# Kernel optimization log

Measured on AMD Instinct MI355X. Metric: run time of the kernel, lower is better.

Reference implementation:

```python
import jax, jax.numpy as jnp
import numpy as np

T, B, N, KALL, F, ORD, DIN, H, NH, HD, DE, DOUT = 4, 4, 16384, 4, 16384, 3, 4, 64, 4, 16, 4, 64


def setup_inputs() -> dict:
    key = jax.random.key(0)
    ks = jax.random.split(key, 32)
    p = lambda k, shape: (jax.random.normal(k, shape) * 0.1).astype(jnp.float32)
    indices = jax.random.randint(ks[0], (F, ORD), 0, N, dtype=jnp.int32)
    cnt = jnp.zeros((N,), jnp.float32).at[indices.reshape(-1)].add(1.0)
    nnz = jnp.maximum(cnt, 1.0)  # per-node nonzero count (avoid div-by-zero)
    return {
        "h": p(ks[1], (B, N, H)),
        "h_global": p(ks[2], (B, KALL, DOUT)),
        "x": p(ks[3], (T, B, N, DIN)),
        "extra": p(ks[4], (T, B, KALL, DE)),
        "dones": jax.random.bernoulli(ks[5], 0.1, (T, B)),
        "indices": indices,
        "nnz": nnz,
        # GRU cell params (flax GRUCell layout: i-dense with bias, h-dense no bias except n-gate)
        "Wi": p(ks[6], (DIN, 3 * H)), "bi": p(ks[7], (3 * H,)),
        "Wh": p(ks[8], (H, 3 * H)), "bhn": p(ks[9], (H,)),
        # MultiHeadAttention params
        "Wq": p(ks[10], (H, NH, HD)), "bq": p(ks[11], (NH, HD)),
        "Wk": p(ks[12], (H, NH, HD)), "bk": p(ks[13], (NH, HD)),
        "Wv": p(ks[14], (H, NH, HD)), "bv": p(ks[15], (NH, HD)),
        "Wo": p(ks[16], (NH, HD, H)), "bo": p(ks[17], (H,)),
        # output MLP (logit head) and value head
        "W1": p(ks[18], (H + DE, DOUT)), "b1": p(ks[19], (DOUT,)),
        "W2": p(ks[20], (DOUT, 1)), "b2": p(ks[21], (1,)),
        "Wv1": p(ks[22], (H + DE, 1)), "bv1": p(ks[23], (1,)),
    }


def reference(h, h_global, x, extra, dones, indices, nnz,
              Wi, bi, Wh, bhn, Wq, bq, Wk, bk, Wv, bv, Wo, bo,
              W1, b1, W2, b2, Wv1, bv1):
    Hd = Wh.shape[0]

    def gru_step(carry, inp):
        xt, dt = inp  # xt: [B,N,din], dt: [B]
        c = jnp.where(dt[:, None, None], jnp.zeros_like(carry), carry)
        gi = xt @ Wi + bi          # [B,N,3H]
        gh = c @ Wh                # [B,N,3H]
        r = jax.nn.sigmoid(gi[..., :Hd] + gh[..., :Hd])
        z = jax.nn.sigmoid(gi[..., Hd:2 * Hd] + gh[..., Hd:2 * Hd])
        n = jnp.tanh(gi[..., 2 * Hd:] + r * (gh[..., 2 * Hd:] + bhn))
        new = (1.0 - z) * n + z * c
        return new, new

    h_fin, hs = jax.lax.scan(gru_step, h, (x, dones))  # hs: [T,B,N,H]

    # gather per-factor neighbor hidden states
    g = jnp.take(hs, indices, axis=2)  # [T,B,F,ord,H]
    q = jnp.einsum('tbfkh,hnd->tbfknd', g, Wq) + bq
    kk = jnp.einsum('tbfkh,hnd->tbfknd', g, Wk) + bk
    vv = jnp.einsum('tbfkh,hnd->tbfknd', g, Wv) + bv
    scale = 1.0 / np.sqrt(q.shape[-1]).astype(np.float32)
    att = jax.nn.softmax(jnp.einsum('tbfqnd,tbfknd->tbfnqk', q * scale, kk), axis=-1)
    o = jnp.einsum('tbfnqk,tbfknd->tbfqnd', att, vv)
    a = jnp.einsum('tbfknd,ndh->tbfkh', o, Wo) + bo  # [T,B,F,ord,H]

    Tn, Bn = a.shape[0], a.shape[1]
    Nn = nnz.shape[0]
    a_flat = a.reshape(Tn, Bn, -1, a.shape[-1])  # [T,B,F*ord,H]
    # segment-sum scatter back to nodes, normalized by nnz
    y = jnp.zeros((Tn, Bn, Nn, a.shape[-1]), a.dtype).at[:, :, indices.reshape(-1), :].add(a_flat)
    y = y / nnz[None, None, :, None]

    Kall = extra.shape[2]
    N0 = Nn // Kall
    ypi = y.reshape(Tn, Bn, Kall, N0, y.shape[-1])
    y_global = jnp.mean(ypi, axis=3)                       # [T,B,K,H]
    z_global = jnp.concatenate((y_global, extra), axis=3)  # [T,B,K,H+DE]
    extra_t = jnp.broadcast_to(extra[:, :, :, None, :], (Tn, Bn, Kall, N0, extra.shape[-1]))
    z = jnp.concatenate((ypi, extra_t), axis=4).reshape(Tn, Bn, Nn, -1)
    value = (z_global @ Wv1 + bv1).sum(axis=2)             # [T,B,1]
    logit = (jax.nn.relu(z @ W1 + b1) @ W2 + b2).squeeze(axis=3)  # [T,B,N]
    return h_fin, h_global, logit, value.squeeze(axis=-1)
```

## Files before the change

### kernel.cpp

```cpp
#include <hip/hip_runtime.h>
#include <hip/hip_bf16.h>

#define T_ 4
#define B_ 4
#define N_ 16384
#define KALL_ 4
#define F_ 16384
#define ORD_ 3
#define DIN_ 4
#define H_ 64
#define H3_ 192
#define DE_ 4
#define STR 72
#define NE_ 49152

typedef __attribute__((ext_vector_type(8))) short s16x8;
typedef __attribute__((ext_vector_type(4))) float f32x4;
typedef __attribute__((ext_vector_type(2))) float f32x2;
typedef unsigned long long u64;

static __device__ __forceinline__ float b2f(unsigned short u) {
  union { unsigned u; float f; } x; x.u = ((unsigned)u) << 16; return x.f;
}
static __device__ __forceinline__ unsigned short f2b(float f) {
  __hip_bfloat16 h = __float2bfloat16(f);
  union { __hip_bfloat16 h; unsigned short u; } x; x.h = h; return x.u;
}
static __device__ __forceinline__ float sigm_fast(float v) {
  return __builtin_amdgcn_rcpf(1.f + __expf(-v));
}
static __device__ __forceinline__ float tanh_fast(float v) {
  float e = __expf(2.f * v);
  return 1.f - 2.f * __builtin_amdgcn_rcpf(e + 1.f);
}

__global__ __launch_bounds__(256) void k_csr_count(
    const int* __restrict__ idx, int* __restrict__ cnt) {
  int e = blockIdx.x * 256 + threadIdx.x;
  if (e < NE_) atomicAdd(&cnt[idx[e]], 1);
}
__global__ __launch_bounds__(256) void k_csr_scan(
    const int* __restrict__ cnt, int* __restrict__ offs, int* __restrict__ cursor) {
  __shared__ int part[256];
  __shared__ int base[256];
  int t = threadIdx.x;
  int s = 0;
  for (int j = 0; j < 64; ++j) s += cnt[t * 64 + j];
  part[t] = s;
  __syncthreads();
  if (t == 0) {
    int run = 0;
    for (int i = 0; i < 256; ++i) { base[i] = run; run += part[i]; }
  }
  __syncthreads();
  int run = base[t];
  for (int j = 0; j < 64; ++j) {
    offs[t * 64 + j] = run;
    cursor[t * 64 + j] = run;
    run += cnt[t * 64 + j];
  }
  if (t == 255) offs[N_] = run;
}
__global__ __launch_bounds__(256) void k_csr_fill(
    const int* __restrict__ idx, int* __restrict__ cursor, int* __restrict__ elist) {
  int e = blockIdx.x * 256 + threadIdx.x;
  if (e < NE_) {
    int pos = atomicAdd(&cursor[idx[e]], 1);
    elist[pos] = e;
  }
}

__global__ __launch_bounds__(256) void k_prep_wh(
    const float* __restrict__ Wh, unsigned short* __restrict__ whTg) {
  int i = blockIdx.x * 256 + threadIdx.x;
  int rr = i >> 6, k = i & 63;
  int ct = rr >> 4, c = rr & 15;
  int g = ct >> 2, cg = ct & 3;
  whTg[i] = f2b(Wh[k * H3_ + g * 64 + 4 * c + cg]);
}

__global__ __launch_bounds__(256) void k_prep_wa(
    const float* __restrict__ Wq, const float* __restrict__ Wk,
    const float* __restrict__ Wv, const float* __restrict__ Wo,
    unsigned short* __restrict__ wT) {
  int i = blockIdx.x * 256 + threadIdx.x;
  int m = i >> 12, col = (i >> 6) & 63, k = i & 63;
  const float* Wm = (m == 0) ? Wq : (m == 1) ? Wk : (m == 2) ? Wv : Wo;
  wT[i] = f2b(Wm[k * 64 + col]);
}

__global__ __launch_bounds__(256) void k_gru(
    const float* __restrict__ h0,
    const float* __restrict__ x,
    const int* __restrict__ dones,
    const unsigned short* __restrict__ whTg,
    const float* __restrict__ Wi,
    const float* __restrict__ bi,
    const float* __restrict__ bhn,
    unsigned short* __restrict__ hs,
    float* __restrict__ hfin)
{
  __shared__ __align__(16) short whT[H3_ * 72];
  __shared__ __align__(16) short carry[H_ * 72];
  __shared__ float wiS[5 * H3_];

  const int tid = threadIdx.x;
  const int lane = tid & 63;
  const int w = tid >> 6;
  const int c15 = lane & 15;
  const int hi4 = lane >> 4;
  const int bid = blockIdx.x;
  const int b = bid >> 8;
  const int nbase = (bid & 255) * 64;
  const int hb = 4 * c15;

#pragma unroll
  for (int c = 0; c < 6; ++c) {
    int lin = (c * 256 + tid) * 8;
    int row = lin >> 6, col = lin & 63;
    *(s16x8*)&whT[row * 72 + col] = *(const s16x8*)&whTg[lin];
  }
  for (int i = tid; i < 5 * H3_; i += 256)
    wiS[i] = (i < 4 * H3_) ? Wi[i] : bi[i - 4 * H3_];

  f32x4 cf[4];
#pragma unroll
  for (int r = 0; r < 4; ++r) {
    int row = 16 * w + 4 * hi4 + r;
    cf[r] = *(const f32x4*)&h0[(size_t)(b * N_ + nbase + row) * H_ + hb];
    u64 pk = 0;
#pragma unroll
    for (int e = 0; e < 4; ++e) pk |= (u64)f2b(cf[r][e]) << (16 * e);
    *(u64*)&carry[row * 72 + hb] = pk;
  }

  float bhnr[4];
#pragma unroll
  for (int cg = 0; cg < 4; ++cg) bhnr[cg] = bhn[hb + cg];

  unsigned dmask = 0;
  {
    bool word = true;
#pragma unroll
    for (int i = 0; i < 16; ++i) {
      int v = dones[i];
      if (v != 0 && v != 1 && v != 0x3F800000) word = false;
    }
#pragma unroll
    for (int t = 0; t < T_; ++t) {
      int tb = t * B_ + b;
      bool d = word ? (dones[tb] != 0) : (((const unsigned char*)dones)[tb] != 0);
      if (d) dmask |= (1u << t);
    }
  }

  __syncthreads();

  const int rowA = 16 * w + c15;
  for (int t = 0; t < T_; ++t) {
    if ((dmask >> t) & 1u) {
#pragma unroll
      for (int r = 0; r < 4; ++r) {
        cf[r] = (f32x4){0.f, 0.f, 0.f, 0.f};
        *(u64*)&carry[(16 * w + 4 * hi4 + r) * 72 + hb] = 0ull;
      }
    }

    s16x8 af0 = *(const s16x8*)&carry[rowA * 72 + hi4 * 8];
    s16x8 af1 = *(const s16x8*)&carry[rowA * 72 + 32 + hi4 * 8];

    f32x4 xv[4];
#pragma unroll
    for (int r = 0; r < 4; ++r) {
      const int node = nbase + 16 * w + 4 * hi4 + r;
      xv[r] = *(const f32x4*)&x[(size_t)((t * B_ + b) * N_ + node) * DIN_];
    }

#pragma unroll
    for (int hh = 0; hh < 2; ++hh) {
      f32x4 acc[6];
#pragma unroll
      for (int j = 0; j < 6; ++j) acc[j] = (f32x4){0.f, 0.f, 0.f, 0.f};
#pragma unroll
      for (int j = 0; j < 6; ++j) {
        const int ct = (j >> 1) * 4 + 2 * hh + (j & 1);
        acc[j] = __builtin_amdgcn_mfma_f32_16x16x32_bf16(
            af0, *(const s16x8*)&whT[(16 * ct + c15) * 72 + hi4 * 8], acc[j], 0, 0, 0);
      }
#pragma unroll
      for (int j = 0; j < 6; ++j) {
        const int ct = (j >> 1) * 4 + 2 * hh + (j & 1);
        acc[j] = __builtin_amdgcn_mfma_f32_16x16x32_bf16(
            af1, *(const s16x8*)&whT[(16 * ct + c15) * 72 + 32 + hi4 * 8], acc[j], 0, 0, 0);
      }
      const int hb2 = hb + 2 * hh;
#pragma unroll
      for (int r = 0; r < 4; ++r) {
        f32x2 gi[3];
#pragma unroll
        for (int g = 0; g < 3; ++g) {
          f32x2 s = *(const f32x2*)&wiS[4 * H3_ + g * 64 + hb2];
#pragma unroll
          for (int kk = 0; kk < 4; ++kk) {
            f32x2 wv = *(const f32x2*)&wiS[kk * H3_ + g * 64 + hb2];
            s += xv[r][kk] * wv;
          }
          gi[g] = s;
        }
#pragma unroll
        for (int c2 = 0; c2 < 2; ++c2) {
          const int cg = 2 * hh + c2;
          float rg = sigm_fast(gi[0][c2] + acc[c2][r]);
          float zg = sigm_fast(gi[1][c2] + acc[2 + c2][r]);
          float ng = tanh_fast(gi[2][c2] + rg * (acc[4 + c2][r] + bhnr[cg]));
          float nc = zg * (cf[r][cg] - ng) + ng;
          cf[r][cg] = nc;
        }
      }
    }

#pragma unroll
    for (int r = 0; r < 4; ++r) {
      const int row = 16 * w + 4 * hi4 + r;
      const int node = nbase + row;
      u64 pk = 0;
#pragma unroll
      for (int e = 0; e < 4; ++e) pk |= (u64)f2b(cf[r][e]) << (16 * e);
      *(u64*)&hs[(size_t)((t * B_ + b) * N_ + node) * H_ + hb] = pk;
      *(u64*)&carry[row * 72 + hb] = pk;
      if (t == T_ - 1)
        *(f32x4*)&hfin[(size_t)(b * N_ + node) * H_ + hb] = cf[r];
    }
  }
}

__global__ __launch_bounds__(256) void k_attn(
    const int tb0,
    const unsigned short* __restrict__ hs,
    const int* __restrict__ indices,
    const unsigned short* __restrict__ wT,
    const float* __restrict__ bq, const float* __restrict__ bk,
    const float* __restrict__ bv, const float* __restrict__ bo,
    unsigned short* __restrict__ a_edge)
{
  __shared__ __align__(16) unsigned short bufrag[3072];
  __shared__ __align__(8)  unsigned short qkvs[9792];
  __shared__ float biasf[4][64];
  __shared__ int idxs[48];

  const int tid = threadIdx.x;
  const int lane = tid & 63;
  const int w = tid >> 6;
  const int c15 = lane & 15;
  const int hi4 = lane >> 4;
  const int bid = blockIdx.x;
  const int slice = bid >> 10;
  const int fch = bid & 1023;
  const int col = 16 * w + c15;
  const int swz = (c15 ^ (hi4 << 2));

  if (tid < 48) idxs[tid] = indices[fch * 48 + tid];
  if (tid < 64) {
    biasf[0][tid] = bq[tid];
    biasf[1][tid] = bk[tid];
    biasf[2][tid] = bv[tid];
    biasf[3][tid] = bo[tid];
  }

  s16x8 wB[3][2], wB3[2];
#pragma unroll
  for (int m = 0; m < 3; ++m)
#pragma unroll
    for (int ks = 0; ks < 2; ++ks)
      wB[m][ks] = *(const s16x8*)&wT[(m * 64 + col) * 64 + ks * 32 + hi4 * 8];
#pragma unroll
  for (int ks = 0; ks < 2; ++ks)
    wB3[ks] = *(const s16x8*)&wT[(3 * 64 + col) * 64 + ks * 32 + hi4 * 8];
  __syncthreads();

  const size_t hbase = (size_t)(tb0 + slice) * N_;
  u64 pf[3];
#pragma unroll
  for (int k = 0; k < 3; ++k) {
    int idx = k * 256 + tid, row = idx >> 4, g = idx & 15;
    pf[k] = *(const u64*)&hs[(hbase + idxs[row]) * H_ + g * 4];
  }
#pragma unroll
  for (int k = 0; k < 3; ++k) {
    int idx = k * 256 + tid, row = idx >> 4, g = idx & 15;
    int rt = row >> 4, cr = row & 15;
    int ks = g >> 3, h5 = (g >> 1) & 3, j = (g & 1) * 4;
    int cr2 = cr ^ (h5 << 2);
    *(u64*)&bufrag[((rt * 2 + ks) << 9) + ((h5 * 16 + cr2) << 3) + j] = pf[k];
  }
  __syncthreads();

  s16x8 afr[3][2];
#pragma unroll
  for (int rt = 0; rt < 3; ++rt)
#pragma unroll
    for (int ks = 0; ks < 2; ++ks)
      afr[rt][ks] = *(const s16x8*)&bufrag[((rt * 2 + ks) << 9) + ((hi4 * 16 + swz) << 3)];
#pragma unroll
  for (int m = 0; m < 3; ++m) {
    float bias = biasf[m][col];
    float scl = (m == 0) ? 0.25f : 1.f;
#pragma unroll
    for (int rt = 0; rt < 3; ++rt) {
      f32x4 acc = (f32x4){0.f, 0.f, 0.f, 0.f};
      acc = __builtin_amdgcn_mfma_f32_16x16x32_bf16(afr[rt][0], wB[m][0], acc, 0, 0, 0);
      acc = __builtin_amdgcn_mfma_f32_16x16x32_bf16(afr[rt][1], wB[m][1], acc, 0, 0, 0);
#pragma unroll
      for (int r = 0; r < 4; ++r) {
        int row = 16 * rt + hi4 * 4 + r;
        qkvs[m * 3264 + row * 68 + col] = f2b((acc[r] + bias) * scl);
      }
    }
  }
  __syncthreads();

  {
    int f = tid >> 4, head = (tid >> 2) & 3, dq = tid & 3;
    int colb = head * 16 + dq * 4;
    float qv[3][4], kv[3][4], vv[3][4];
#pragma unroll
    for (int qi = 0; qi < 3; ++qi) {
      int base = (3 * f + qi) * 68 + colb;
      u64 uq = *(const u64*)&qkvs[base];
      u64 uk = *(const u64*)&qkvs[3264 + base];
      u64 uv = *(const u64*)&qkvs[6528 + base];
#pragma unroll
      for (int e = 0; e < 4; ++e) {
        qv[qi][e] = b2f((unsigned short)(uq >> (16 * e)));
        kv[qi][e] = b2f((unsigned short)(uk >> (16 * e)));
        vv[qi][e] = b2f((unsigned short)(uv >> (16 * e)));
      }
    }
    float s[3][3];
#pragma unroll
    for (int qi = 0; qi < 3; ++qi)
#pragma unroll
      for (int ki = 0; ki < 3; ++ki) {
        float a = qv[qi][0] * kv[ki][0] + qv[qi][1] * kv[ki][1]
                + qv[qi][2] * kv[ki][2] + qv[qi][3] * kv[ki][3];
        a += __shfl_xor(a, 1, 64);
        a += __shfl_xor(a, 2, 64);
        s[qi][ki] = a;
      }
    const int ks2 = colb >> 5, h5b = (colb >> 3) & 3, jb = colb & 7;
#pragma unroll
    for (int qi = 0; qi < 3; ++qi) {
      float mx = fmaxf(s[qi][0], fmaxf(s[qi][1], s[qi][2]));
      float e0 = __expf(s[qi][0] - mx), e1 = __expf(s[qi][1] - mx), e2 = __expf(s[qi][2] - mx);
      float inv = 1.f / (e0 + e1 + e2);
      e0 *= inv; e1 *= inv; e2 *= inv;
      int row = 3 * f + qi;
      int rt = row >> 4, cr2 = (row & 15) ^ (h5b << 2);
      u64 pack = 0;
#pragma unroll
      for (int e = 0; e < 4; ++e) {
        float o = e0 * vv[0][e] + e1 * vv[1][e] + e2 * vv[2][e];
        pack |= (u64)f2b(o) << (16 * e);
      }
      *(u64*)&bufrag[((rt * 2 + ks2) << 9) + ((h5b * 16 + cr2) << 3) + jb] = pack;
    }
  }
  __syncthreads();

  {
    const float bo_ = biasf[3][col];
    const size_t abase = (size_t)slice * NE_ + (size_t)fch * 48;
#pragma unroll
    for (int rt = 0; rt < 3; ++rt) {
      s16x8 o0 = *(const s16x8*)&bufrag[((rt * 2 + 0) << 9) + ((hi4 * 16 + swz) << 3)];
      s16x8 o1 = *(const s16x8*)&bufrag[((rt * 2 + 1) << 9) + ((hi4 * 16 + swz) << 3)];
      f32x4 acc = (f32x4){0.f, 0.f, 0.f, 0.f};
      acc = __builtin_amdgcn_mfma_f32_16x16x32_bf16(o0, wB3[0], acc, 0, 0, 0);
      acc = __builtin_amdgcn_mfma_f32_16x16x32_bf16(o1, wB3[1], acc, 0, 0, 0);
#pragma unroll
      for (int r = 0; r < 4; ++r) {
        int row = 16 * rt + hi4 * 4 + r;
        a_edge[(abase + row) * H_ + col] = f2b(acc[r] + bo_);
      }
    }
  }
}

__global__ __launch_bounds__(256) void k_head(
    const int tb0,
    const unsigned short* __restrict__ a_edge,
    const int* __restrict__ offs, const int* __restrict__ elist,
    const float* __restrict__ nnz,
    const float* __restrict__ extra,
    const float* __restrict__ W1, const float* __restrict__ b1,
    const float* __restrict__ W2, const float* __restrict__ b2,
    float* __restrict__ yg,
    float* __restrict__ logit)
{
  __shared__ short w1T[64 * STR];
  __shared__ short arow[64 * STR];
  __shared__ int offsS[65];
  __shared__ int eidS[512];
  __shared__ float hEx[64];
  __shared__ float w2s[64];
  __shared__ float red[4][64];

  const int tid = threadIdx.x;
  const int lane = tid & 63;
  const int w = tid >> 6;
  const int c15 = lane & 15;
  const int hi4 = lane >> 4;
  const int bid = blockIdx.x;
  const int ls = bid >> 8;
  const int tb = tb0 + ls;
  const int nbase = (bid & 255) * 64;
  const int kall = nbase >> 12;

  for (int i = tid; i < 4096; i += 256) {
    int k = i >> 6, colc = i & 63;
    w1T[colc * STR + k] = (short)f2b(W1[i]);
  }
  if (tid < 65) offsS[tid] = offs[nbase + tid];
  if (tid < 64) {
    float s = b1[tid];
#pragma unroll
    for (int e = 0; e < 4; ++e)
      s += extra[(tb * KALL_ + kall) * DE_ + e] * W1[(64 + e) * 64 + tid];
    hEx[tid] = s;
    w2s[tid] = W2[tid];
  }
  const int ebeg = offs[nbase];
  const int ecnt = offs[nbase + 64] - ebeg;
  const bool fast = (ecnt <= 512);
  if (tid == 0) eidS[0] = 0;
  if (fast) {
    for (int j = tid; j < ecnt; j += 256) eidS[j] = elist[ebeg + j];
  }
  __syncthreads();

  const size_t ebase = (size_t)ls * NE_;
  float accp = 0.f;
  if (fast) {
    for (int r = w; r < 64; r += 4) {
      const int beg = offsS[r] - ebeg, end = offsS[r + 1] - ebeg;
      float s = 0.f;
#pragma unroll
      for (int u = 0; u < 8; ++u) {
        int p = beg + u;
        bool valid = p < end;
        int pc = valid ? p : 0;
        float v = b2f(a_edge[(ebase + eidS[pc]) * H_ + lane]);
        s += valid ? v : 0.f;
      }
      for (int p = beg + 8; p < end; ++p)
        s += b2f(a_edge[(ebase + eidS[p]) * H_ + lane]);
      float val = s / fmaxf((float)(end - beg), 1.f);
      accp += val;
      arow[r * STR + lane] = (short)f2b(val);
    }
  } else {
    for (int r = w; r < 64; r += 4) {
      const int beg = offsS[r], end = offsS[r + 1];
      float s = 0.f;
      for (int p = beg; p < end; ++p)
        s += b2f(a_edge[(ebase + elist[p]) * H_ + lane]);
      float val = s / fmaxf((float)(end - beg), 1.f);
      accp += val;
      arow[r * STR + lane] = (short)f2b(val);
    }
  }
  red[w][lane] = accp;
  __syncthreads();

  f32x4 acc[4];
#pragma unroll
  for (int ct = 0; ct < 4; ++ct) acc[ct] = (f32x4){0.f, 0.f, 0.f, 0.f};
#pragma unroll
  for (int ks = 0; ks < 2; ++ks) {
    int kb = ks * 32 + hi4 * 8;
    s16x8 af = *(const s16x8*)&arow[(16 * w + c15) * STR + kb];
#pragma unroll
    for (int ct = 0; ct < 4; ++ct) {
      s16x8 bfr = *(const s16x8*)&w1T[(16 * ct + c15) * STR + kb];
      acc[ct] = __builtin_amdgcn_mfma_f32_16x16x32_bf16(af, bfr, acc[ct], 0, 0, 0);
    }
  }
  const float b2v = b2[0];
#pragma unroll
  for (int r = 0; r < 4; ++r) {
    float s = 0.f;
#pragma unroll
    for (int ct = 0; ct < 4; ++ct) {
      int colc = 16 * ct + c15;
      s += fmaxf(acc[ct][r] + hEx[colc], 0.f) * w2s[colc];
    }
    s += __shfl_xor(s, 1, 64);
    s += __shfl_xor(s, 2, 64);
    s += __shfl_xor(s, 4, 64);
    s += __shfl_xor(s, 8, 64);
    if (c15 == 0)
      logit[tb * N_ + nbase + 16 * w + hi4 * 4 + r] = s + b2v;
  }
  if (tid < 64) {
    float sv = red[0][tid] + red[1][tid] + red[2][tid] + red[3][tid];
    atomicAdd(&yg[(tb * KALL_ + kall) * H_ + tid], sv);
  }
}

__global__ __launch_bounds__(256) void k_final(
    const float* __restrict__ yg,
    const float* __restrict__ extra,
    const float* __restrict__ Wv1, const float* __restrict__ bv1,
    const float* __restrict__ hg_in,
    float* __restrict__ value_out,
    float* __restrict__ hg_out)
{
  const int tid = threadIdx.x;
  if (tid < 16) {
    const float bv = bv1[0];
    float v = 0.f;
    for (int kall = 0; kall < 4; ++kall) {
      float s = bv;
      for (int hh = 0; hh < 64; ++hh)
        s += (yg[(tid * KALL_ + kall) * H_ + hh] * (1.f / 4096.f)) * Wv1[hh];
      for (int e = 0; e < 4; ++e)
        s += extra[(tid * KALL_ + kall) * DE_ + e] * Wv1[64 + e];
      v += s;
    }
    value_out[tid] = v;
  }
  for (int i = tid; i < 1024; i += 256) hg_out[i] = hg_in[i];
}

extern "C" void kernel_launch(void* const* d_in, const int* in_sizes, int n_in,
                              void* d_out, int out_size, void* d_ws, size_t ws_size,
                              hipStream_t stream)
{
  (void)in_sizes; (void)n_in; (void)out_size; (void)ws_size;
  const float* h0    = (const float*)d_in[0];
  const float* hg    = (const float*)d_in[1];
  const float* x     = (const float*)d_in[2];
  const float* extra = (const float*)d_in[3];
  const int*   dn    = (const int*)d_in[4];
  const int*   idx   = (const int*)d_in[5];
  const float* nnz   = (const float*)d_in[6];
  const float* Wi    = (const float*)d_in[7];
  const float* bi    = (const float*)d_in[8];
  const float* Wh    = (const float*)d_in[9];
  const float* bhn   = (const float*)d_in[10];
  const float* Wq    = (const float*)d_in[11];
  const float* bq    = (const float*)d_in[12];
  const float* Wk    = (const float*)d_in[13];
  const float* bk    = (const float*)d_in[14];
  const float* Wv    = (const float*)d_in[15];
  const float* bv    = (const float*)d_in[16];
  const float* Wo    = (const float*)d_in[17];
  const float* bo    = (const float*)d_in[18];
  const float* W1    = (const float*)d_in[19];
  const float* b1    = (const float*)d_in[20];
  const float* W2    = (const float*)d_in[21];
  const float* b2    = (const float*)d_in[22];
  const float* Wv1   = (const float*)d_in[23];
  const float* bv1   = (const float*)d_in[24];

  float* out = (float*)d_out;
  float* out_hfin  = out;
  float* out_hg    = out + 4194304;
  float* out_logit = out + 4195328;
  float* out_value = out + 4457472;

  char* wsb = (char*)d_ws;
  float*          yg     = (float*)wsb;
  int*            cnt    = (int*)(wsb + 16384);
  int*            offs   = (int*)(wsb + 81920);
  int*            cursor = (int*)(wsb + 147584);
  int*            elist  = (int*)(wsb + 213120);
  unsigned short* whTg   = (unsigned short*)(wsb + 409728);
  unsigned short* wT     = (unsigned short*)(wsb + 434304);
  unsigned short* hs     = (unsigned short*)(wsb + 524288);
  unsigned short* a_edge = (unsigned short*)(wsb + 34078720);

  hipMemsetAsync(wsb, 0, 81920, stream);
  k_csr_count<<<192, 256, 0, stream>>>(idx, cnt);
  k_csr_scan<<<1, 256, 0, stream>>>(cnt, offs, cursor);
  k_csr_fill<<<192, 256, 0, stream>>>(idx, cursor, elist);
  k_prep_wh<<<48, 256, 0, stream>>>(Wh, whTg);
  k_prep_wa<<<64, 256, 0, stream>>>(Wq, Wk, Wv, Wo, wT);
  k_gru<<<1024, 256, 0, stream>>>(h0, x, dn, whTg, Wi, bi, bhn, hs, out_hfin);
  for (int half = 0; half < 2; ++half) {
    const int tb0 = half * 8;
    k_attn<<<8192, 256, 0, stream>>>(tb0, hs, idx, wT, bq, bk, bv, bo, a_edge);
    k_head<<<2048, 256, 0, stream>>>(tb0, a_edge, offs, elist, nnz, extra,
                                     W1, b1, W2, b2, yg, out_logit);
  }
  k_final<<<1, 256, 0, stream>>>(yg, extra, Wv1, bv1, hg, out_value, out_hg);
}
```

Measured before the change: 338.4 us.

## Make attention kernel persistent over time slices with prefetch, fuse prep kernels

The attention kernel now launches one block per edge chunk and loops over the 8 (t,b) slices itself. It loads the weights, biases and gather indices once and prefetches the next slice's gathered hidden rows while the current slice computes. Q and K are kept in fp32 shared memory, which drops a bf16 round-trip. The CSR count and the two weight-prep kernels are merged into one launch to cut launch overhead. In exchange, the grid shrinks from 8192 to 1024 blocks, which lowers available parallelism and latency hiding, and the larger fp32 LDS buffers may reduce occupancy.

```diff
diff --git a/kernel.cpp b/kernel.cpp
--- a/kernel.cpp
+++ b/kernel.cpp
@@ -34,11 +34,30 @@
   return 1.f - 2.f * __builtin_amdgcn_rcpf(e + 1.f);
 }
 
-__global__ __launch_bounds__(256) void k_csr_count(
-    const int* __restrict__ idx, int* __restrict__ cnt) {
-  int e = blockIdx.x * 256 + threadIdx.x;
-  if (e < NE_) atomicAdd(&cnt[idx[e]], 1);
-}
+__global__ __launch_bounds__(256) void k_prep(
+    const int* __restrict__ idx, int* __restrict__ cnt,
+    const float* __restrict__ Wh, unsigned short* __restrict__ whTg,
+    const float* __restrict__ Wq, const float* __restrict__ Wk,
+    const float* __restrict__ Wv, const float* __restrict__ Wo,
+    unsigned short* __restrict__ wT) {
+  const int b = blockIdx.x, tid = threadIdx.x;
+  if (b < 192) {
+    int e = b * 256 + tid;
+    if (e < NE_) atomicAdd(&cnt[idx[e]], 1);
+  } else if (b < 240) {
+    int i = (b - 192) * 256 + tid;
+    int rr = i >> 6, k = i & 63;
+    int ct = rr >> 4, c = rr & 15;
+    int g = ct >> 2, cg = ct & 3;
+    whTg[i] = f2b(Wh[k * H3_ + g * 64 + 4 * c + cg]);
+  } else {
+    int i = (b - 240) * 256 + tid;
+    int m = i >> 12, col = (i >> 6) & 63, k = i & 63;
+    const float* Wm = (m == 0) ? Wq : (m == 1) ? Wk : (m == 2) ? Wv : Wo;
+    wT[i] = f2b(Wm[k * 64 + col]);
+  }
+}
+
 __global__ __launch_bounds__(256) void k_csr_scan(
     const int* __restrict__ cnt, int* __restrict__ offs, int* __restrict__ cursor) {
   __shared__ int part[256];
@@ -68,25 +87,6 @@
     int pos = atomicAdd(&cursor[idx[e]], 1);
     elist[pos] = e;
   }
-}
-
-__global__ __launch_bounds__(256) void k_prep_wh(
-    const float* __restrict__ Wh, unsigned short* __restrict__ whTg) {
-  int i = blockIdx.x * 256 + threadIdx.x;
-  int rr = i >> 6, k = i & 63;
-  int ct = rr >> 4, c = rr & 15;
-  int g = ct >> 2, cg = ct & 3;
-  whTg[i] = f2b(Wh[k * H3_ + g * 64 + 4 * c + cg]);
-}
-
-__global__ __launch_bounds__(256) void k_prep_wa(
-    const float* __restrict__ Wq, const float* __restrict__ Wk,
-    const float* __restrict__ Wv, const float* __restrict__ Wo,
-    unsigned short* __restrict__ wT) {
-  int i = blockIdx.x * 256 + threadIdx.x;
-  int m = i >> 12, col = (i >> 6) & 63, k = i & 63;
-  const float* Wm = (m == 0) ? Wq : (m == 1) ? Wk : (m == 2) ? Wv : Wo;
-  wT[i] = f2b(Wm[k * 64 + col]);
 }
 
 __global__ __launch_bounds__(256) void k_gru(
@@ -244,8 +244,9 @@
     unsigned short* __restrict__ a_edge)
 {
   __shared__ __align__(16) unsigned short bufrag[3072];
-  __shared__ __align__(8)  unsigned short qkvs[9792];
-  __shared__ float biasf[4][64];
+  __shared__ __align__(16) float qs[48 * 68];
+  __shared__ __align__(16) float ksh[48 * 68];
+  __shared__ __align__(8)  unsigned short vs[48 * 68];
   __shared__ int idxs[48];
 
   const int tid = threadIdx.x;
@@ -254,18 +255,10 @@
   const int c15 = lane & 15;
   const int hi4 = lane >> 4;
   const int bid = blockIdx.x;
-  const int slice = bid >> 10;
-  const int fch = bid & 1023;
   const int col = 16 * w + c15;
   const int swz = (c15 ^ (hi4 << 2));
 
-  if (tid < 48) idxs[tid] = indices[fch * 48 + tid];
-  if (tid < 64) {
-    biasf[0][tid] = bq[tid];
-    biasf[1][tid] = bk[tid];
-    biasf[2][tid] = bv[tid];
-    biasf[3][tid] = bo[tid];
-  }
+  if (tid < 48) idxs[tid] = indices[bid * 48 + tid];
 
   s16x8 wB[3][2], wB3[2];
 #pragma unroll
@@ -276,111 +269,133 @@
 #pragma unroll
   for (int ks = 0; ks < 2; ++ks)
     wB3[ks] = *(const s16x8*)&wT[(3 * 64 + col) * 64 + ks * 32 + hi4 * 8];
+  const float bq_c = bq[col], bk_c = bk[col], bv_c = bv[col], bo_c = bo[col];
   __syncthreads();
 
-  const size_t hbase = (size_t)(tb0 + slice) * N_;
+  const int grow = tid >> 4, gg = tid & 15;
+  const int gks = gg >> 3, gh5 = (gg >> 1) & 3, gj = (gg & 1) * 4;
+  size_t goff[3];
+  int boff[3];
+#pragma unroll
+  for (int k = 0; k < 3; ++k) {
+    goff[k] = (size_t)idxs[grow + k * 16] * H_ + gg * 4;
+    int cr2 = grow ^ (gh5 << 2);
+    boff[k] = ((k * 2 + gks) << 9) + ((gh5 * 16 + cr2) << 3) + gj;
+  }
+
   u64 pf[3];
-#pragma unroll
-  for (int k = 0; k < 3; ++k) {
-    int idx = k * 256 + tid, row = idx >> 4, g = idx & 15;
-    pf[k] = *(const u64*)&hs[(hbase + idxs[row]) * H_ + g * 4];
-  }
-#pragma unroll
-  for (int k = 0; k < 3; ++k) {
-    int idx = k * 256 + tid, row = idx >> 4, g = idx & 15;
-    int rt = row >> 4, cr = row & 15;
-    int ks = g >> 3, h5 = (g >> 1) & 3, j = (g & 1) * 4;
-    int cr2 = cr ^ (h5 << 2);
-    *(u64*)&bufrag[((rt * 2 + ks) << 9) + ((h5 * 16 + cr2) << 3) + j] = pf[k];
-  }
-  __syncthreads();
-
-  s16x8 afr[3][2];
-#pragma unroll
-  for (int rt = 0; rt < 3; ++rt)
-#pragma unroll
-    for (int ks = 0; ks < 2; ++ks)
-      afr[rt][ks] = *(const s16x8*)&bufrag[((rt * 2 + ks) << 9) + ((hi4 * 16 + swz) << 3)];
-#pragma unroll
-  for (int m = 0; m < 3; ++m) {
-    float bias = biasf[m][col];
-    float scl = (m == 0) ? 0.25f : 1.f;
+  {
+    const unsigned short* hp = hs + (size_t)tb0 * (N_ * H_);
+#pragma unroll
+    for (int k = 0; k < 3; ++k) pf[k] = *(const u64*)&hp[goff[k]];
+  }
+
+  for (int it = 0; it < 8; ++it) {
+    __syncthreads();
+#pragma unroll
+    for (int k = 0; k < 3; ++k) *(u64*)&bufrag[boff[k]] = pf[k];
+    __syncthreads();
+
+    s16x8 afr[3][2];
+#pragma unroll
+    for (int rt = 0; rt < 3; ++rt)
+#pragma unroll
+      for (int ks = 0; ks < 2; ++ks)
+        afr[rt][ks] = *(const s16x8*)&bufrag[((rt * 2 + ks) << 9) + ((hi4 * 16 + swz) << 3)];
 #pragma unroll
     for (int rt = 0; rt < 3; ++rt) {
-      f32x4 acc = (f32x4){0.f, 0.f, 0.f, 0.f};
-      acc = __builtin_amdgcn_mfma_f32_16x16x32_bf16(afr[rt][0], wB[m][0], acc, 0, 0, 0);
-      acc = __builtin_amdgcn_mfma_f32_16x16x32_bf16(afr[rt][1], wB[m][1], acc, 0, 0, 0);
-#pragma unroll
-      for (int r = 0; r < 4; ++r) {
-        int row = 16 * rt + hi4 * 4 + r;
-        qkvs[m * 3264 + row * 68 + col] = f2b((acc[r] + bias) * scl);
-      }
-    }
-  }
-  __syncthreads();
-
-  {
-    int f = tid >> 4, head = (tid >> 2) & 3, dq = tid & 3;
-    int colb = head * 16 + dq * 4;
-    float qv[3][4], kv[3][4], vv[3][4];
-#pragma unroll
-    for (int qi = 0; qi < 3; ++qi) {
-      int base = (3 * f + qi) * 68 + colb;
-      u64 uq = *(const u64*)&qkvs[base];
-      u64 uk = *(const u64*)&qkvs[3264 + base];
-      u64 uv = *(const u64*)&qkvs[6528 + base];
-#pragma unroll
-      for (int e = 0; e < 4; ++e) {
-        qv[qi][e] = b2f((unsigned short)(uq >> (16 * e)));
-        kv[qi][e] = b2f((unsigned short)(uk >> (16 * e)));
-        vv[qi][e] = b2f((unsigned short)(uv >> (16 * e)));
-      }
-    }
-    float s[3][3];
-#pragma unroll
-    for (int qi = 0; qi < 3; ++qi)
-#pragma unroll
-      for (int ki = 0; ki < 3; ++ki) {
-        float a = qv[qi][0] * kv[ki][0] + qv[qi][1] * kv[ki][1]
-                + qv[qi][2] * kv[ki][2] + qv[qi][3] * kv[ki][3];
-        a += __shfl_xor(a, 1, 64);
-        a += __shfl_xor(a, 2, 64);
-        s[qi][ki] = a;
-      }
-    const int ks2 = colb >> 5, h5b = (colb >> 3) & 3, jb = colb & 7;
-#pragma unroll
-    for (int qi = 0; qi < 3; ++qi) {
-      float mx = fmaxf(s[qi][0], fmaxf(s[qi][1], s[qi][2]));
-      float e0 = __expf(s[qi][0] - mx), e1 = __expf(s[qi][1] - mx), e2 = __expf(s[qi][2] - mx);
-      float inv = 1.f / (e0 + e1 + e2);
-      e0 *= inv; e1 *= inv; e2 *= inv;
-      int row = 3 * f + qi;
-      int rt = row >> 4, cr2 = (row & 15) ^ (h5b << 2);
-      u64 pack = 0;
-#pragma unroll
-      for (int e = 0; e < 4; ++e) {
-        float o = e0 * vv[0][e] + e1 * vv[1][e] + e2 * vv[2][e];
-        pack |= (u64)f2b(o) << (16 * e);
-      }
-      *(u64*)&bufrag[((rt * 2 + ks2) << 9) + ((h5b * 16 + cr2) << 3) + jb] = pack;
-    }
-  }
-  __syncthreads();
-
-  {
-    const float bo_ = biasf[3][col];
-    const size_t abase = (size_t)slice * NE_ + (size_t)fch * 48;
+      f32x4 aq = (f32x4){0.f, 0.f, 0.f, 0.f};
+      aq = __builtin_amdgcn_mfma_f32_16x16x32_bf16(afr[rt][0], wB[0][0], aq, 0, 0, 0);
+      aq = __builtin_amdgcn_mfma_f32_16x16x32_bf16(afr[rt][1], wB[0][1], aq, 0, 0, 0);
+#pragma unroll
+      for (int r = 0; r < 4; ++r)
+        qs[(16 * rt + hi4 * 4 + r) * 68 + col] = (aq[r] + bq_c) * 0.25f;
+    }
 #pragma unroll
     for (int rt = 0; rt < 3; ++rt) {
-      s16x8 o0 = *(const s16x8*)&bufrag[((rt * 2 + 0) << 9) + ((hi4 * 16 + swz) << 3)];
-      s16x8 o1 = *(const s16x8*)&bufrag[((rt * 2 + 1) << 9) + ((hi4 * 16 + swz) << 3)];
-      f32x4 acc = (f32x4){0.f, 0.f, 0.f, 0.f};
-      acc = __builtin_amdgcn_mfma_f32_16x16x32_bf16(o0, wB3[0], acc, 0, 0, 0);
-      acc = __builtin_amdgcn_mfma_f32_16x16x32_bf16(o1, wB3[1], acc, 0, 0, 0);
-#pragma unroll
-      for (int r = 0; r < 4; ++r) {
-        int row = 16 * rt + hi4 * 4 + r;
-        a_edge[(abase + row) * H_ + col] = f2b(acc[r] + bo_);
+      f32x4 ak = (f32x4){0.f, 0.f, 0.f, 0.f};
+      ak = __builtin_amdgcn_mfma_f32_16x16x32_bf16(afr[rt][0], wB[1][0], ak, 0, 0, 0);
+      ak = __builtin_amdgcn_mfma_f32_16x16x32_bf16(afr[rt][1], wB[1][1], ak, 0, 0, 0);
+#pragma unroll
+      for (int r = 0; r < 4; ++r)
+        ksh[(16 * rt + hi4 * 4 + r) * 68 + col] = ak[r] + bk_c;
+    }
+#pragma unroll
+    for (int rt = 0; rt < 3; ++rt) {
+      f32x4 av = (f32x4){0.f, 0.f, 0.f, 0.f};
+      av = __builtin_amdgcn_mfma_f32_16x16x32_bf16(afr[rt][0], wB[2][0], av, 0, 0, 0);
+      av = __builtin_amdgcn_mfma_f32_16x16x32_bf16(afr[rt][1], wB[2][1], av, 0, 0, 0);
+#pragma unroll
+      for (int r = 0; r < 4; ++r)
+        vs[(16 * rt + hi4 * 4 + r) * 68 + col] = f2b(av[r] + bv_c);
+    }
+    if (it < 7) {
+      const unsigned short* hp = hs + (size_t)(tb0 + it + 1) * (N_ * H_);
+#pragma unroll
+      for (int k = 0; k < 3; ++k) pf[k] = *(const u64*)&hp[goff[k]];
+    }
+    __syncthreads();
+
+    {
+      int f = tid >> 4, head = (tid >> 2) & 3, dq = tid & 3;
+      int colb = head * 16 + dq * 4;
+      f32x4 qv[3], kv[3];
+      float vv[3][4];
+#pragma unroll
+      for (int qi = 0; qi < 3; ++qi) {
+        int base = (3 * f + qi) * 68 + colb;
+        qv[qi] = *(const f32x4*)&qs[base];
+        kv[qi] = *(const f32x4*)&ksh[base];
+        u64 uv = *(const u64*)&vs[base];
+#pragma unroll
+        for (int e = 0; e < 4; ++e)
+          vv[qi][e] = b2f((unsigned short)(uv >> (16 * e)));
+      }
+      float s[3][3];
+#pragma unroll
+      for (int qi = 0; qi < 3; ++qi)
+#pragma unroll
+        for (int ki = 0; ki < 3; ++ki) {
+          float a = qv[qi][0] * kv[ki][0] + qv[qi][1] * kv[ki][1]
+                  + qv[qi][2] * kv[ki][2] + qv[qi][3] * kv[ki][3];
+          a += __shfl_xor(a, 1, 64);
+          a += __shfl_xor(a, 2, 64);
+          s[qi][ki] = a;
+        }
+      const int ks2 = colb >> 5, h5b = (colb >> 3) & 3, jb = colb & 7;
+#pragma unroll
+      for (int qi = 0; qi < 3; ++qi) {
+        float mx = fmaxf(s[qi][0], fmaxf(s[qi][1], s[qi][2]));
+        float e0 = __expf(s[qi][0] - mx), e1 = __expf(s[qi][1] - mx), e2 = __expf(s[qi][2] - mx);
+        float inv = 1.f / (e0 + e1 + e2);
+        e0 *= inv; e1 *= inv; e2 *= inv;
+        int row = 3 * f + qi;
+        int rt = row >> 4, cr2 = (row & 15) ^ (h5b << 2);
+        u64 pack = 0;
+#pragma unroll
+        for (int e = 0; e < 4; ++e) {
+          float o = e0 * vv[0][e] + e1 * vv[1][e] + e2 * vv[2][e];
+          pack |= (u64)f2b(o) << (16 * e);
+        }
+        *(u64*)&bufrag[((rt * 2 + ks2) << 9) + ((h5b * 16 + cr2) << 3) + jb] = pack;
+      }
+    }
+    __syncthreads();
+
+    {
+      const size_t abase = (size_t)it * NE_ + (size_t)bid * 48;
+#pragma unroll
+      for (int rt = 0; rt < 3; ++rt) {
+        s16x8 o0 = *(const s16x8*)&bufrag[((rt * 2 + 0) << 9) + ((hi4 * 16 + swz) << 3)];
+        s16x8 o1 = *(const s16x8*)&bufrag[((rt * 2 + 1) << 9) + ((hi4 * 16 + swz) << 3)];
+        f32x4 acc = (f32x4){0.f, 0.f, 0.f, 0.f};
+        acc = __builtin_amdgcn_mfma_f32_16x16x32_bf16(o0, wB3[0], acc, 0, 0, 0);
+        acc = __builtin_amdgcn_mfma_f32_16x16x32_bf16(o1, wB3[1], acc, 0, 0, 0);
+#pragma unroll
+        for (int r = 0; r < 4; ++r) {
+          int row = 16 * rt + hi4 * 4 + r;
+          a_edge[(abase + row) * H_ + col] = f2b(acc[r] + bo_c);
+        }
       }
     }
   }
@@ -581,15 +596,13 @@
   unsigned short* a_edge = (unsigned short*)(wsb + 34078720);
 
   hipMemsetAsync(wsb, 0, 81920, stream);
-  k_csr_count<<<192, 256, 0, stream>>>(idx, cnt);
+  k_prep<<<304, 256, 0, stream>>>(idx, cnt, Wh, whTg, Wq, Wk, Wv, Wo, wT);
   k_csr_scan<<<1, 256, 0, stream>>>(cnt, offs, cursor);
   k_csr_fill<<<192, 256, 0, stream>>>(idx, cursor, elist);
-  k_prep_wh<<<48, 256, 0, stream>>>(Wh, whTg);
-  k_prep_wa<<<64, 256, 0, stream>>>(Wq, Wk, Wv, Wo, wT);
   k_gru<<<1024, 256, 0, stream>>>(h0, x, dn, whTg, Wi, bi, bhn, hs, out_hfin);
   for (int half = 0; half < 2; ++half) {
     const int tb0 = half * 8;
-    k_attn<<<8192, 256, 0, stream>>>(tb0, hs, idx, wT, bq, bk, bv, bo, a_edge);
+    k_attn<<<1024, 256, 0, stream>>>(tb0, hs, idx, wT, bq, bk, bv, bo, a_edge);
     k_head<<<2048, 256, 0, stream>>>(tb0, a_edge, offs, elist, nnz, extra,
                                      W1, b1, W2, b2, yg, out_logit);
   }
```

Measured after the change: 334.3 us. Within noise of the previous version (-1.2%).
